# Kernel optimization log

Hardware: AMD Instinct MI355X
Metric: run time of the kernel (lower is better)

The kernel has to match this reference:

```python
import jax, jax.numpy as jnp
import numpy as np

N, E, H = 5000, 40000, 8
DIMS = [(258, 512), (516, 256), (262, 128), (136, 20)]  # (in_feature, out_feature) per GATDeformer


def setup_inputs() -> dict:
    key = jax.random.key(0)
    ks = jax.random.split(key, 10)
    s = 0.05
    data = jax.random.normal(ks[0], (N, 10), jnp.float32)
    src = jax.random.randint(ks[1], (E,), 0, N)
    off = jax.random.randint(ks[2], (E,), 1, N)
    edge_idx = jnp.stack([src, (src + off) % N]).astype(jnp.int32)  # no self loops by construction
    inp = {
        'data': data,
        'edge_idx': edge_idx,
        'W0': jax.random.normal(ks[3], (10, 256), jnp.float32) * s,
        'b0': jnp.zeros((256,), jnp.float32),
    }
    for i, (din, dout) in enumerate(DIMS, start=1):
        k = jax.random.split(ks[3 + i], 3)
        inp[f'W{i}'] = jax.random.normal(k[0], (din, H * dout), jnp.float32) * s
        inp[f'asrc{i}'] = jax.random.normal(k[1], (H, dout), jnp.float32) * s
        inp[f'adst{i}'] = jax.random.normal(k[2], (H, dout), jnp.float32) * s
        inp[f'bias{i}'] = jnp.zeros((dout,), jnp.float32)
    return inp


def _gat(x, src, dst, W, a_s, a_d, b):
    """PyG GATConv (concat=False): returns (mean-over-heads output + bias, alpha [E',H])."""
    Hh, C = a_s.shape
    h = (x @ W).reshape(N, Hh, C)                               # [N,H,C]
    e_s = jnp.einsum('nhc,hc->nh', h, a_s)                      # [N,H]
    e_d = jnp.einsum('nhc,hc->nh', h, a_d)
    logits = jax.nn.leaky_relu(e_s[src] + e_d[dst], 0.2)        # [E',H]
    m = jax.ops.segment_max(logits, dst, num_segments=N)        # segment softmax over incoming edges
    ex = jnp.exp(logits - m[dst])
    alpha = ex / jax.ops.segment_sum(ex, dst, num_segments=N)[dst]
    out = jax.ops.segment_sum(alpha[:, :, None] * h[src], dst, num_segments=N)  # [N,H,C]
    return out.mean(axis=1) + b, alpha


def _deformer(af, src, dst, W, a_s, a_d, b):
    # find_boundary on the layer input features
    up, down = af[:, 0] == 1.0, af[:, 0] == 0.0
    left, right = af[:, 1] == 0.0, af[:, 1] == 1.0
    feat, alpha = _gat(af, src, dst, W, a_s, a_d, b)
    coord = af[:, :2]
    # second propagate: alpha*0.2 reused to aggregate source coordinates, then mean over heads
    msg = (alpha * 0.2)[:, :, None] * coord[src][:, None, :]    # [E',H,2]
    oc = jax.ops.segment_sum(msg, dst, num_segments=N).mean(axis=1)
    # fix_boundary (sequential overwrite order: up then down, left then right)
    c0 = jnp.where(down, 0.0, jnp.where(up, 1.0, oc[:, 0]))
    c1 = jnp.where(right, 1.0, jnp.where(left, 0.0, oc[:, 1]))
    return jnp.stack([c0, c1], axis=1), jax.nn.selu(feat)


def reference(data, edge_idx, W0, b0, W1, asrc1, adst1, bias1, W2, asrc2, adst2, bias2, W3, asrc3, adst3, bias3, W4, asrc4, adst4, bias4):
    sl = jnp.arange(N, dtype=edge_idx.dtype)
    src = jnp.concatenate([edge_idx[0], sl])   # GATConv add_self_loops=True
    dst = jnp.concatenate([edge_idx[1], sl])
    coord = data[:, :2]
    feat = jax.nn.selu(data @ W0 + b0)
    c1_, f1 = _deformer(jnp.concatenate([coord, feat], 1), src, dst, W1, asrc1, adst1, bias1)
    c2_, f2 = _deformer(jnp.concatenate([c1_, coord, f1], 1), src, dst, W2, asrc2, adst2, bias2)
    c3_, f3 = _deformer(jnp.concatenate([c2_, c1_, coord, f2], 1), src, dst, W3, asrc3, adst3, bias3)
    c4_, _ = _deformer(jnp.concatenate([c3_, c2_, c1_, coord, f3], 1), src, dst, W4, asrc4, adst4, bias4)
    return c4_
```

## Files before the change

### kernel.cpp

```cpp
#include <hip/hip_runtime.h>

#define N_NODES 5000
#define NH 8

typedef unsigned short u16;
typedef short bf16x8 __attribute__((ext_vector_type(8)));
typedef float f32x4 __attribute__((ext_vector_type(4)));

static __device__ __forceinline__ float selu_f(float x) {
    const float sc = 1.0507009873554805f;
    const float al = 1.6732632423543772f;
    return x > 0.f ? sc * x : sc * al * (__expf(x) - 1.f);
}

static __device__ __forceinline__ u16 f2bf(float x) {
    union { float f; unsigned u; } v; v.f = x;
    unsigned r = v.u + 0x7fff + ((v.u >> 16) & 1);
    return (u16)(r >> 16);
}

static __device__ __forceinline__ float bf2f(unsigned hi16) {
    union { unsigned u; float f; } v; v.u = hi16 << 16;
    return v.f;
}

__global__ void k_count(const int* __restrict__ ei, int* cnt, int E, int Esz) {
    int e = blockIdx.x * 256 + threadIdx.x;
    if (e >= Esz) return;
    int dst = (e < E) ? ei[E + e] : (e - E);
    atomicAdd(&cnt[dst], 1);
}

__global__ void k_scan(const int* __restrict__ cnt, int* __restrict__ rowp, int n) {
    __shared__ int ps[256];
    int t = threadIdx.x;
    int per = (n + 255) / 256;
    int b = t * per;
    int s = 0;
    for (int i = 0; i < per; ++i) { int idx = b + i; if (idx < n) s += cnt[idx]; }
    ps[t] = s;
    __syncthreads();
    for (int off = 1; off < 256; off <<= 1) {
        int v = (t >= off) ? ps[t - off] : 0;
        __syncthreads();
        ps[t] += v;
        __syncthreads();
    }
    int run = (t == 0) ? 0 : ps[t - 1];
    for (int i = 0; i < per; ++i) {
        int idx = b + i;
        if (idx < n) { rowp[idx] = run; run += cnt[idx]; }
    }
    if (t == 255) rowp[n] = run;
}

__global__ void k_fill(const int* __restrict__ ei, const int* __restrict__ rowp,
                       int* cur, int* ssrc, int E, int Esz) {
    int e = blockIdx.x * 256 + threadIdx.x;
    if (e >= Esz) return;
    int src, dst;
    if (e < E) { src = ei[e]; dst = ei[E + e]; }
    else       { src = e - E; dst = src; }
    int pos = rowp[dst] + atomicAdd(&cur[dst], 1);
    ssrc[pos] = src;
}

__global__ void k_feat0(const float* __restrict__ data, const float* __restrict__ W0,
                        const float* __restrict__ b0, float* __restrict__ f0,
                        float* __restrict__ c0) {
    int n = blockIdx.x;
    int t = threadIdx.x;
    __shared__ float d[10];
    if (t < 10) d[t] = data[n * 10 + t];
    __syncthreads();
    float acc = b0[t];
    #pragma unroll
    for (int k = 0; k < 10; ++k) acc += d[k] * W0[k * 256 + t];
    f0[(size_t)n * 256 + t] = selu_f(acc);
    if (t < 2) c0[n * 2 + t] = d[t];
}

__global__ void k_foldall(const float* W1, const float* W2, const float* W3, const float* W4,
                          const float* s1, const float* s2, const float* s3, const float* s4,
                          const float* d1, const float* d2, const float* d3, const float* d4,
                          float* __restrict__ fsAll, float* __restrict__ fdAll) {
    const int Ks[4] = {258, 516, 262, 136};
    const int Cs[4] = {512, 256, 128, 20};
    int li = blockIdx.y;
    int k = blockIdx.x;
    if (k >= Ks[li]) return;
    const float* W  = (li == 0) ? W1 : (li == 1) ? W2 : (li == 2) ? W3 : W4;
    const float* as = (li == 0) ? s1 : (li == 1) ? s2 : (li == 2) ? s3 : s4;
    const float* ad = (li == 0) ? d1 : (li == 1) ? d2 : (li == 2) ? d3 : d4;
    int C = Cs[li];
    int lane = threadIdx.x;
    float s[8] = {0.f,0.f,0.f,0.f,0.f,0.f,0.f,0.f};
    float d[8] = {0.f,0.f,0.f,0.f,0.f,0.f,0.f,0.f};
    const float* wr = W + (size_t)k * 8 * C;
    for (int c = lane; c < C; c += 64) {
        #pragma unroll
        for (int h = 0; h < 8; ++h) {
            float w = wr[h * C + c];
            s[h] += w * as[h * C + c];
            d[h] += w * ad[h * C + c];
        }
    }
    #pragma unroll
    for (int off = 32; off >= 1; off >>= 1) {
        #pragma unroll
        for (int h = 0; h < 8; ++h) {
            s[h] += __shfl_xor(s[h], off);
            d[h] += __shfl_xor(d[h], off);
        }
    }
    if (lane == 0) {
        float* fo = fsAll + (size_t)li * 516 * 8 + k * 8;
        float* go = fdAll + (size_t)li * 516 * 8 + k * 8;
        #pragma unroll
        for (int h = 0; h < 8; ++h) { fo[h] = s[h]; go[h] = d[h]; }
    }
}

__global__ __launch_bounds__(256) void k_wtrall(const float* W1, const float* W2, const float* W3,
                                                u16* T1, u16* T2, u16* T3) {
    const int Ks[3] = {258, 516, 262};
    const int Cs[3] = {512, 256, 128};
    const int Kps[3] = {288, 544, 288};
    int li = blockIdx.z;
    int C = Cs[li], K = Ks[li], Kp = Kps[li], KK = 8 * Kp;
    int c0 = blockIdx.x * 32;
    int j0 = blockIdx.y * 32;
    if (c0 >= C || j0 >= KK) return;
    const float* W = (li == 0) ? W1 : (li == 1) ? W2 : W3;
    u16* Wt2 = (li == 0) ? T1 : (li == 1) ? T2 : T3;
    __shared__ float tile[32][33];
    int h = j0 / Kp, k0 = j0 % Kp;
    int tid = threadIdx.x;
    for (int idx = tid; idx < 1024; idx += 256) {
        int kr = idx >> 5, cc = idx & 31;
        int gk = k0 + kr;
        tile[kr][cc] = (gk < K) ? W[(size_t)gk * (8 * C) + h * C + c0 + cc] : 0.f;
    }
    __syncthreads();
    for (int idx = tid; idx < 1024; idx += 256) {
        int cr = idx >> 5, kc = idx & 31;
        Wt2[(size_t)(c0 + cr) * KK + j0 + kc] = f2bf(tile[kc][cr]);
    }
}

__global__ __launch_bounds__(256) void k_mf(const float* p0, const float* p1,
                                            const float* p2, const float* p3, int np,
                                            const float* __restrict__ fplain,
                                            const float* __restrict__ facc,
                                            const float* __restrict__ biasp,
                                            int split, int MN, int FC, int K, int Kp,
                                            const float* __restrict__ fs,
                                            const float* __restrict__ fd,
                                            u16* __restrict__ afb,
                                            float* __restrict__ es, float* __restrict__ ed) {
    int n = blockIdx.x, t = threadIdx.x;
    float pes[8] = {0.f,0.f,0.f,0.f,0.f,0.f,0.f,0.f};
    float ped[8] = {0.f,0.f,0.f,0.f,0.f,0.f,0.f,0.f};
    u16* rowb = afb + (size_t)n * Kp;
    for (int cf = t; cf < FC; cf += 256) {
        float v;
        if (biasp) {
            float s = 0.f;
            for (int z = 0; z < split; ++z)
                s += facc[(size_t)z * MN + (size_t)n * FC + cf];
            v = selu_f(s * 0.125f + biasp[cf]);
        } else {
            v = fplain[(size_t)n * FC + cf];
        }
        int c = 2 * np + cf;
        rowb[c] = f2bf(v);
        const float* fsr = fs + c * 8;
        const float* fdr = fd + c * 8;
        #pragma unroll
        for (int h = 0; h < 8; ++h) { pes[h] += v * fsr[h]; ped[h] += v * fdr[h]; }
    }
    if (t < 2 * np) {
        const float* p = (t < 2) ? p0 : (t < 4) ? p1 : (t < 6) ? p2 : p3;
        float v = p[n * 2 + (t & 1)];
        rowb[t] = f2bf(v);
        #pragma unroll
        for (int h = 0; h < 8; ++h) { pes[h] += v * fs[t * 8 + h]; ped[h] += v * fd[t * 8 + h]; }
    }
    for (int c = K + t; c < Kp; c += 256) rowb[c] = 0;
    #pragma unroll
    for (int off = 32; off >= 1; off >>= 1) {
        #pragma unroll
        for (int h = 0; h < 8; ++h) {
            pes[h] += __shfl_xor(pes[h], off);
            ped[h] += __shfl_xor(ped[h], off);
        }
    }
    __shared__ float red[4][16];
    int wv = t >> 6, ln = t & 63;
    if (ln == 0) {
        #pragma unroll
        for (int h = 0; h < 8; ++h) { red[wv][h] = pes[h]; red[wv][8 + h] = ped[h]; }
    }
    __syncthreads();
    if (t < 16) {
        float s = red[0][t] + red[1][t] + red[2][t] + red[3][t];
        if (t < 8) es[n * 8 + t] = s;
        else       ed[n * 8 + (t - 8)] = s;
    }
}

template <int S32>
__global__ __launch_bounds__(256) void k_gag(const float* __restrict__ es,
                            const float* __restrict__ ed,
                            const int* __restrict__ rowp, const int* __restrict__ ssrc,
                            const float* __restrict__ cprev, const u16* __restrict__ afb,
                            u16* __restrict__ g, float* __restrict__ cnext, int Kp) {
    __shared__ int   ls[128];
    __shared__ float la[128 * 8];
    __shared__ float lc0[128], lc1[128], lw[128];
    __shared__ float linv[8];
    int n = blockIdx.x, t = threadIdx.x;
    int s0 = rowp[n];
    int deg = rowp[n + 1] - s0;
    if (deg > 128) deg = 128;
    for (int i = t; i < deg; i += 256) {
        int src = ssrc[s0 + i];
        ls[i] = src;
        lc0[i] = cprev[src * 2];
        lc1[i] = cprev[src * 2 + 1];
    }
    __syncthreads();
    for (int i = t; i < deg * 8; i += 256) {
        int e = i >> 3, h = i & 7;
        float x = es[ls[e] * 8 + h] + ed[n * 8 + h];
        la[i] = x > 0.f ? x : 0.2f * x;
    }
    __syncthreads();
    if (t < 8) {
        float m = -1e30f;
        for (int e = 0; e < deg; ++e) m = fmaxf(m, la[e * 8 + t]);
        float s = 0.f;
        for (int e = 0; e < deg; ++e) {
            float v = __expf(la[e * 8 + t] - m);
            la[e * 8 + t] = v;
            s += v;
        }
        linv[t] = 1.f / s;
    }
    __syncthreads();
    for (int i = t; i < deg; i += 256) {
        float w = 0.f;
        #pragma unroll
        for (int h = 0; h < 8; ++h) w += la[i * 8 + h] * linv[h];
        lw[i] = w;
    }
    int nW = Kp >> 1;
    float acc[8][2 * S32];
    #pragma unroll
    for (int h = 0; h < 8; ++h)
        #pragma unroll
        for (int s = 0; s < 2 * S32; ++s) acc[h][s] = 0.f;
    int e = 0;
    for (; e + 1 < deg; e += 2) {
        const unsigned* r0 = (const unsigned*)(afb + (size_t)ls[e] * Kp);
        const unsigned* r1 = (const unsigned*)(afb + (size_t)ls[e + 1] * Kp);
        unsigned v0[S32], v1[S32];
        #pragma unroll
        for (int s = 0; s < S32; ++s) {
            int w = t + 256 * s;
            v0[s] = (w < nW) ? r0[w] : 0u;
            v1[s] = (w < nW) ? r1[w] : 0u;
        }
        float a0[8], a1[8];
        #pragma unroll
        for (int h = 0; h < 8; ++h) { a0[h] = la[e * 8 + h]; a1[h] = la[(e + 1) * 8 + h]; }
        #pragma unroll
        for (int s = 0; s < S32; ++s) {
            float x0 = bf2f(v0[s] & 0xffff), y0 = bf2f(v0[s] >> 16);
            float x1 = bf2f(v1[s] & 0xffff), y1 = bf2f(v1[s] >> 16);
            #pragma unroll
            for (int h = 0; h < 8; ++h) {
                acc[h][2 * s]     += a0[h] * x0 + a1[h] * x1;
                acc[h][2 * s + 1] += a0[h] * y0 + a1[h] * y1;
            }
        }
    }
    if (e < deg) {
        const unsigned* r0 = (const unsigned*)(afb + (size_t)ls[e] * Kp);
        unsigned v0[S32];
        #pragma unroll
        for (int s = 0; s < S32; ++s) {
            int w = t + 256 * s;
            v0[s] = (w < nW) ? r0[w] : 0u;
        }
        float a0[8];
        #pragma unroll
        for (int h = 0; h < 8; ++h) a0[h] = la[e * 8 + h];
        #pragma unroll
        for (int s = 0; s < S32; ++s) {
            float x0 = bf2f(v0[s] & 0xffff), y0 = bf2f(v0[s] >> 16);
            #pragma unroll
            for (int h = 0; h < 8; ++h) {
                acc[h][2 * s]     += a0[h] * x0;
                acc[h][2 * s + 1] += a0[h] * y0;
            }
        }
    }
    unsigned* grw = (unsigned*)(g + (size_t)n * 8 * Kp);
    #pragma unroll
    for (int s = 0; s < S32; ++s) {
        int w = t + 256 * s;
        if (w < nW) {
            #pragma unroll
            for (int h = 0; h < 8; ++h) {
                float iv = linv[h];
                unsigned lo = f2bf(acc[h][2 * s] * iv);
                unsigned hi = f2bf(acc[h][2 * s + 1] * iv);
                grw[h * nW + w] = lo | (hi << 16);
            }
        }
    }
    __syncthreads();
    if (t == 0) {
        float oc0 = 0.f, oc1 = 0.f;
        for (int i = 0; i < deg; ++i) { oc0 += lw[i] * lc0[i]; oc1 += lw[i] * lc1[i]; }
        oc0 *= 0.025f; oc1 *= 0.025f;
        float a0 = cprev[n * 2], a1 = cprev[n * 2 + 1];
        cnext[n * 2]     = (a0 == 0.f) ? 0.f : ((a0 == 1.f) ? 1.f : oc0);
        cnext[n * 2 + 1] = (a1 == 1.f) ? 1.f : ((a1 == 0.f) ? 0.f : oc1);
    }
}

__global__ __launch_bounds__(256) void k_gemm_s(const u16* __restrict__ A,
                                                const u16* __restrict__ Bt,
                                                float* __restrict__ facc,
                                                int M, int KK, int NC, int kchunk) {
    __shared__ u16 As[128 * 32];
    __shared__ u16 Bs[128 * 32];
    int tid = threadIdx.x;
    int wave = tid >> 6, lane = tid & 63;
    int bm = blockIdx.y * 128, bn = blockIdx.x * 128, z = blockIdx.z;
    int kbeg = z * kchunk, kend = min(KK, kbeg + kchunk);
    int wm = (wave >> 1) * 64, wn = (wave & 1) * 64;
    int l16 = lane & 15, q = lane >> 4;
    f32x4 acc[4][4] = {};
    for (int k0 = kbeg; k0 < kend; k0 += 32) {
        #pragma unroll
        for (int it = 0; it < 2; ++it) {
            int seg = tid + it * 256;
            int row = seg >> 2, sq = seg & 3;
            uint4 va = {0u, 0u, 0u, 0u};
            int grow = bm + row;
            if (grow < M) va = *(const uint4*)(A + (size_t)grow * KK + k0 + sq * 8);
            *(uint4*)(As + row * 32 + ((sq ^ (row & 3)) * 8)) = va;
            uint4 vb = *(const uint4*)(Bt + (size_t)(bn + row) * KK + k0 + sq * 8);
            *(uint4*)(Bs + row * 32 + ((sq ^ (row & 3)) * 8)) = vb;
        }
        __syncthreads();
        bf16x8 fa[4], fb[4];
        #pragma unroll
        for (int mi = 0; mi < 4; ++mi) {
            int row = wm + mi * 16 + l16;
            fa[mi] = *(const bf16x8*)(As + row * 32 + ((q ^ (row & 3)) * 8));
            int col = wn + mi * 16 + l16;
            fb[mi] = *(const bf16x8*)(Bs + col * 32 + ((q ^ (col & 3)) * 8));
        }
        #pragma unroll
        for (int mi = 0; mi < 4; ++mi)
            #pragma unroll
            for (int ni = 0; ni < 4; ++ni)
                acc[mi][ni] = __builtin_amdgcn_mfma_f32_16x16x32_bf16(fa[mi], fb[ni], acc[mi][ni], 0, 0, 0);
        __syncthreads();
    }
    float* out = facc + (size_t)z * M * NC;
    #pragma unroll
    for (int mi = 0; mi < 4; ++mi) {
        int row0 = bm + wm + mi * 16 + q * 4;
        #pragma unroll
        for (int ni = 0; ni < 4; ++ni) {
            int col = bn + wn + ni * 16 + l16;
            #pragma unroll
            for (int r = 0; r < 4; ++r) {
                int row = row0 + r;
                if (row < M) out[(size_t)row * NC + col] = acc[mi][ni][r];
            }
        }
    }
}

__global__ void k_final(const float* __restrict__ es, const float* __restrict__ ed,
                        const int* __restrict__ rowp, const int* __restrict__ ssrc,
                        const float* __restrict__ cprev, float* __restrict__ outp) {
    int wid = (blockIdx.x * blockDim.x + threadIdx.x) >> 6;
    int lane = threadIdx.x & 63;
    if (wid >= N_NODES) return;
    int n = wid;
    int s0 = rowp[n], deg = rowp[n + 1] - s0;
    int h = lane & 7, ei = lane >> 3;
    float edh = ed[n * 8 + h];
    float m = -1e30f;
    for (int b = 0; b < deg; b += 8) {
        int e = b + ei;
        if (e < deg) {
            int src = ssrc[s0 + e];
            float x = es[src * 8 + h] + edh;
            x = x > 0.f ? x : 0.2f * x;
            m = fmaxf(m, x);
        }
    }
    m = fmaxf(m, __shfl_xor(m, 8));
    m = fmaxf(m, __shfl_xor(m, 16));
    m = fmaxf(m, __shfl_xor(m, 32));
    float ssum = 0.f;
    for (int b = 0; b < deg; b += 8) {
        int e = b + ei;
        if (e < deg) {
            int src = ssrc[s0 + e];
            float x = es[src * 8 + h] + edh;
            x = x > 0.f ? x : 0.2f * x;
            ssum += __expf(x - m);
        }
    }
    ssum += __shfl_xor(ssum, 8);
    ssum += __shfl_xor(ssum, 16);
    ssum += __shfl_xor(ssum, 32);
    float inv = 1.f / ssum;
    float oc0 = 0.f, oc1 = 0.f;
    for (int b = 0; b < deg; b += 8) {
        int e = b + ei;
        if (e < deg) {
            int src = ssrc[s0 + e];
            float x = es[src * 8 + h] + edh;
            x = x > 0.f ? x : 0.2f * x;
            float w = __expf(x - m) * inv;
            w += __shfl_xor(w, 1);
            w += __shfl_xor(w, 2);
            w += __shfl_xor(w, 4);
            if (h == 0) {
                oc0 += w * cprev[src * 2];
                oc1 += w * cprev[src * 2 + 1];
            }
        }
    }
    oc0 += __shfl_xor(oc0, 8);  oc1 += __shfl_xor(oc1, 8);
    oc0 += __shfl_xor(oc0, 16); oc1 += __shfl_xor(oc1, 16);
    oc0 += __shfl_xor(oc0, 32); oc1 += __shfl_xor(oc1, 32);
    if (lane == 0) {
        oc0 *= 0.025f; oc1 *= 0.025f;
        float a0 = cprev[n * 2], a1 = cprev[n * 2 + 1];
        outp[n * 2]     = (a0 == 0.f) ? 0.f : ((a0 == 1.f) ? 1.f : oc0);
        outp[n * 2 + 1] = (a1 == 1.f) ? 1.f : ((a1 == 0.f) ? 0.f : oc1);
    }
}

extern "C" void kernel_launch(void* const* d_in, const int* in_sizes, int n_in,
                              void* d_out, int out_size, void* d_ws, size_t ws_size,
                              hipStream_t stream) {
    const float* data = (const float*)d_in[0];
    const int* ei = (const int*)d_in[1];
    const float* W0 = (const float*)d_in[2];
    const float* b0 = (const float*)d_in[3];
    int E = in_sizes[1] / 2;
    int Esz = E + N_NODES;

    char* wp = (char*)d_ws;
    size_t off = 0;
    auto alloc = [&](size_t bytes) {
        void* p = wp + off;
        off += (bytes + 1023) & ~(size_t)1023;
        return p;
    };
    u16*   g     = (u16*)alloc((size_t)N_NODES * 8 * 576 * 2);
    u16*   T1    = (u16*)alloc((size_t)512 * 8 * 288 * 2);
    u16*   T2    = (u16*)alloc((size_t)256 * 8 * 544 * 2);
    u16*   T3    = (u16*)alloc((size_t)128 * 8 * 288 * 2);
    float* facc  = (float*)alloc((size_t)N_NODES * 2048 * 4);
    float* fA    = (float*)alloc((size_t)N_NODES * 256 * 4);
    u16*   afb   = (u16*)alloc((size_t)N_NODES * 576 * 2);
    float* es    = (float*)alloc((size_t)N_NODES * 8 * 4);
    float* ebd   = (float*)alloc((size_t)N_NODES * 8 * 4);
    float* fsAll = (float*)alloc((size_t)4 * 516 * 8 * 4);
    float* fdAll = (float*)alloc((size_t)4 * 516 * 8 * 4);
    float* c0    = (float*)alloc(N_NODES * 2 * 4);
    float* c1    = (float*)alloc(N_NODES * 2 * 4);
    float* c2    = (float*)alloc(N_NODES * 2 * 4);
    float* c3    = (float*)alloc(N_NODES * 2 * 4);
    int* cnt  = (int*)alloc(N_NODES * 2 * 4);
    int* cur  = cnt + N_NODES;
    int* rowp = (int*)alloc((N_NODES + 1) * 4);
    int* ssrc = (int*)alloc(Esz * 4);

    hipMemsetAsync(cnt, 0, N_NODES * 2 * 4, stream);
    int gE = (Esz + 255) / 256;
    k_count<<<gE, 256, 0, stream>>>(ei, cnt, E, Esz);
    k_scan<<<1, 256, 0, stream>>>(cnt, rowp, N_NODES);
    k_fill<<<gE, 256, 0, stream>>>(ei, rowp, cur, ssrc, E, Esz);
    k_feat0<<<N_NODES, 256, 0, stream>>>(data, W0, b0, fA, c0);

    struct LP { const float *W, *as, *ad, *bs; int K, C, split; };
    LP L[4] = {
        {(const float*)d_in[4],  (const float*)d_in[5],  (const float*)d_in[6],  (const float*)d_in[7],  258, 512, 4},
        {(const float*)d_in[8],  (const float*)d_in[9],  (const float*)d_in[10], (const float*)d_in[11], 516, 256, 8},
        {(const float*)d_in[12], (const float*)d_in[13], (const float*)d_in[14], (const float*)d_in[15], 262, 128, 8},
        {(const float*)d_in[16], (const float*)d_in[17], (const float*)d_in[18], (const float*)d_in[19], 136, 20, 1},
    };
    k_foldall<<<dim3(516, 4), 64, 0, stream>>>(L[0].W, L[1].W, L[2].W, L[3].W,
                                               L[0].as, L[1].as, L[2].as, L[3].as,
                                               L[0].ad, L[1].ad, L[2].ad, L[3].ad,
                                               fsAll, fdAll);
    k_wtrall<<<dim3(16, 136, 3), 256, 0, stream>>>(L[0].W, L[1].W, L[2].W, T1, T2, T3);

    float* cbuf[4] = {c0, c1, c2, c3};
    u16* Tb[3] = {T1, T2, T3};
    int FC[4] = {256, 512, 256, 128};

    for (int li = 0; li < 4; ++li) {
        LP& lp = L[li];
        const float* p[4] = {nullptr, nullptr, nullptr, nullptr};
        for (int j = 0; j <= li; ++j) p[j] = cbuf[li - j];
        int Kp = ((lp.K + 31) / 32) * 32;
        int KK = 8 * Kp;
        const float* biasp = (li == 0) ? nullptr : L[li - 1].bs;
        int splitp = (li == 0) ? 1 : L[li - 1].split;
        int MNp = N_NODES * FC[li];
        const float* fs = fsAll + (size_t)li * 516 * 8;
        const float* fd = fdAll + (size_t)li * 516 * 8;

        k_mf<<<N_NODES, 256, 0, stream>>>(p[0], p[1], p[2], p[3], li + 1,
                                          fA, facc, biasp, splitp, MNp, FC[li],
                                          lp.K, Kp, fs, fd, afb, es, ebd);
        if (li < 3) {
            if ((Kp >> 1) <= 256)
                k_gag<1><<<N_NODES, 256, 0, stream>>>(es, ebd, rowp, ssrc, cbuf[li], afb,
                                                      g, cbuf[li + 1], Kp);
            else
                k_gag<2><<<N_NODES, 256, 0, stream>>>(es, ebd, rowp, ssrc, cbuf[li], afb,
                                                      g, cbuf[li + 1], Kp);
            k_gemm_s<<<dim3(lp.C / 128, (N_NODES + 127) / 128, lp.split), 256, 0, stream>>>(
                g, Tb[li], facc, N_NODES, KK, lp.C, KK / lp.split);
        } else {
            k_final<<<(N_NODES + 3) / 4, 256, 0, stream>>>(es, ebd, rowp, ssrc, cbuf[3],
                                                           (float*)d_out);
        }
    }
}
```

Before: 381.5 us.

## Fuse first-layer MLP into k_mf, map one wave per node in gather, store split-K partials as bf16

The standalone k_feat0 kernel is removed and its selu(data@W0+b0) is computed inside the layer-1 k_mf pass, dropping one launch and an fp32 intermediate round trip. k_gag now handles four nodes per block with one wave per node, using 64-bit vector loads, and reduces coordinates with a wave shuffle instead of a serial thread-0 loop. Split-K GEMM partials are written as bf16 instead of fp32, halving that traffic. The costs are more bf16 rounding on the accumulated partial sums and a lower in-degree cap (96 instead of 128) in the gather.

```diff
diff --git a/kernel.cpp b/kernel.cpp
--- a/kernel.cpp
+++ b/kernel.cpp
@@ -63,21 +63,6 @@
     else       { src = e - E; dst = src; }
     int pos = rowp[dst] + atomicAdd(&cur[dst], 1);
     ssrc[pos] = src;
-}
-
-__global__ void k_feat0(const float* __restrict__ data, const float* __restrict__ W0,
-                        const float* __restrict__ b0, float* __restrict__ f0,
-                        float* __restrict__ c0) {
-    int n = blockIdx.x;
-    int t = threadIdx.x;
-    __shared__ float d[10];
-    if (t < 10) d[t] = data[n * 10 + t];
-    __syncthreads();
-    float acc = b0[t];
-    #pragma unroll
-    for (int k = 0; k < 10; ++k) acc += d[k] * W0[k * 256 + t];
-    f0[(size_t)n * 256 + t] = selu_f(acc);
-    if (t < 2) c0[n * 2 + t] = d[t];
 }
 
 __global__ void k_foldall(const float* W1, const float* W2, const float* W3, const float* W4,
@@ -150,27 +135,37 @@
 
 __global__ __launch_bounds__(256) void k_mf(const float* p0, const float* p1,
                                             const float* p2, const float* p3, int np,
-                                            const float* __restrict__ fplain,
-                                            const float* __restrict__ facc,
+                                            const float* __restrict__ data,
+                                            const float* __restrict__ W0,
+                                            const float* __restrict__ b0,
+                                            const u16* __restrict__ facc,
                                             const float* __restrict__ biasp,
                                             int split, int MN, int FC, int K, int Kp,
                                             const float* __restrict__ fs,
                                             const float* __restrict__ fd,
                                             u16* __restrict__ afb,
-                                            float* __restrict__ es, float* __restrict__ ed) {
+                                            float* __restrict__ es, float* __restrict__ ed,
+                                            float* __restrict__ c0out) {
     int n = blockIdx.x, t = threadIdx.x;
+    __shared__ float drow[10];
+    bool l1 = (biasp == nullptr);
+    if (l1 && t < 10) drow[t] = data[n * 10 + t];
+    __syncthreads();
     float pes[8] = {0.f,0.f,0.f,0.f,0.f,0.f,0.f,0.f};
     float ped[8] = {0.f,0.f,0.f,0.f,0.f,0.f,0.f,0.f};
     u16* rowb = afb + (size_t)n * Kp;
     for (int cf = t; cf < FC; cf += 256) {
         float v;
-        if (biasp) {
+        if (l1) {
+            v = b0[cf];
+            #pragma unroll
+            for (int k = 0; k < 10; ++k) v += drow[k] * W0[k * 256 + cf];
+            v = selu_f(v);
+        } else {
             float s = 0.f;
             for (int z = 0; z < split; ++z)
-                s += facc[(size_t)z * MN + (size_t)n * FC + cf];
+                s += bf2f(facc[(size_t)z * MN + (size_t)n * FC + cf]);
             v = selu_f(s * 0.125f + biasp[cf]);
-        } else {
-            v = fplain[(size_t)n * FC + cf];
         }
         int c = 2 * np + cf;
         rowb[c] = f2bf(v);
@@ -180,8 +175,14 @@
         for (int h = 0; h < 8; ++h) { pes[h] += v * fsr[h]; ped[h] += v * fdr[h]; }
     }
     if (t < 2 * np) {
-        const float* p = (t < 2) ? p0 : (t < 4) ? p1 : (t < 6) ? p2 : p3;
-        float v = p[n * 2 + (t & 1)];
+        float v;
+        if (l1) {
+            v = drow[t];
+            c0out[n * 2 + t] = v;
+        } else {
+            const float* p = (t < 2) ? p0 : (t < 4) ? p1 : (t < 6) ? p2 : p3;
+            v = p[n * 2 + (t & 1)];
+        }
         rowb[t] = f2bf(v);
         #pragma unroll
         for (int h = 0; h < 8; ++h) { pes[h] += v * fs[t * 8 + h]; ped[h] += v * fd[t * 8 + h]; }
@@ -209,132 +210,147 @@
     }
 }
 
-template <int S32>
+template <int S>
 __global__ __launch_bounds__(256) void k_gag(const float* __restrict__ es,
                             const float* __restrict__ ed,
                             const int* __restrict__ rowp, const int* __restrict__ ssrc,
                             const float* __restrict__ cprev, const u16* __restrict__ afb,
                             u16* __restrict__ g, float* __restrict__ cnext, int Kp) {
-    __shared__ int   ls[128];
-    __shared__ float la[128 * 8];
-    __shared__ float lc0[128], lc1[128], lw[128];
-    __shared__ float linv[8];
-    int n = blockIdx.x, t = threadIdx.x;
+    const int DC = 96;
+    __shared__ int   ls[4][DC];
+    __shared__ float la[4][DC * 8];
+    __shared__ float lc0[4][DC], lc1[4][DC];
+    __shared__ float linv[4][8];
+    int wv = threadIdx.x >> 6, lane = threadIdx.x & 63;
+    int n = blockIdx.x * 4 + wv;
     int s0 = rowp[n];
     int deg = rowp[n + 1] - s0;
-    if (deg > 128) deg = 128;
-    for (int i = t; i < deg; i += 256) {
+    if (deg > DC) deg = DC;
+    for (int i = lane; i < deg; i += 64) {
         int src = ssrc[s0 + i];
-        ls[i] = src;
-        lc0[i] = cprev[src * 2];
-        lc1[i] = cprev[src * 2 + 1];
-    }
-    __syncthreads();
-    for (int i = t; i < deg * 8; i += 256) {
+        ls[wv][i] = src;
+        lc0[wv][i] = cprev[src * 2];
+        lc1[wv][i] = cprev[src * 2 + 1];
+    }
+    __syncthreads();
+    for (int i = lane; i < deg * 8; i += 64) {
         int e = i >> 3, h = i & 7;
-        float x = es[ls[e] * 8 + h] + ed[n * 8 + h];
-        la[i] = x > 0.f ? x : 0.2f * x;
-    }
-    __syncthreads();
-    if (t < 8) {
+        float x = es[ls[wv][e] * 8 + h] + ed[n * 8 + h];
+        la[wv][i] = x > 0.f ? x : 0.2f * x;
+    }
+    __syncthreads();
+    if (lane < 8) {
         float m = -1e30f;
-        for (int e = 0; e < deg; ++e) m = fmaxf(m, la[e * 8 + t]);
+        for (int e = 0; e < deg; ++e) m = fmaxf(m, la[wv][e * 8 + lane]);
         float s = 0.f;
         for (int e = 0; e < deg; ++e) {
-            float v = __expf(la[e * 8 + t] - m);
-            la[e * 8 + t] = v;
+            float v = __expf(la[wv][e * 8 + lane] - m);
+            la[wv][e * 8 + lane] = v;
             s += v;
         }
-        linv[t] = 1.f / s;
-    }
-    __syncthreads();
-    for (int i = t; i < deg; i += 256) {
+        linv[wv][lane] = 1.f / s;
+    }
+    __syncthreads();
+    float pc0 = 0.f, pc1 = 0.f;
+    for (int i = lane; i < deg; i += 64) {
         float w = 0.f;
         #pragma unroll
-        for (int h = 0; h < 8; ++h) w += la[i * 8 + h] * linv[h];
-        lw[i] = w;
-    }
-    int nW = Kp >> 1;
-    float acc[8][2 * S32];
+        for (int h = 0; h < 8; ++h) w += la[wv][i * 8 + h] * linv[wv][h];
+        pc0 += w * lc0[wv][i];
+        pc1 += w * lc1[wv][i];
+    }
+    #pragma unroll
+    for (int o = 32; o >= 1; o >>= 1) { pc0 += __shfl_xor(pc0, o); pc1 += __shfl_xor(pc1, o); }
+    if (lane == 0) {
+        pc0 *= 0.025f; pc1 *= 0.025f;
+        float a0 = cprev[n * 2], a1 = cprev[n * 2 + 1];
+        cnext[n * 2]     = (a0 == 0.f) ? 0.f : ((a0 == 1.f) ? 1.f : pc0);
+        cnext[n * 2 + 1] = (a1 == 1.f) ? 1.f : ((a1 == 0.f) ? 0.f : pc1);
+    }
+    int n64 = Kp >> 2;
+    float acc[8][4 * S];
     #pragma unroll
     for (int h = 0; h < 8; ++h)
         #pragma unroll
-        for (int s = 0; s < 2 * S32; ++s) acc[h][s] = 0.f;
+        for (int j = 0; j < 4 * S; ++j) acc[h][j] = 0.f;
     int e = 0;
     for (; e + 1 < deg; e += 2) {
-        const unsigned* r0 = (const unsigned*)(afb + (size_t)ls[e] * Kp);
-        const unsigned* r1 = (const unsigned*)(afb + (size_t)ls[e + 1] * Kp);
-        unsigned v0[S32], v1[S32];
-        #pragma unroll
-        for (int s = 0; s < S32; ++s) {
-            int w = t + 256 * s;
-            v0[s] = (w < nW) ? r0[w] : 0u;
-            v1[s] = (w < nW) ? r1[w] : 0u;
+        const uint2* r0 = (const uint2*)(afb + (size_t)ls[wv][e] * Kp);
+        const uint2* r1 = (const uint2*)(afb + (size_t)ls[wv][e + 1] * Kp);
+        uint2 v0[S], v1[S];
+        #pragma unroll
+        for (int s = 0; s < S; ++s) {
+            int w = lane + 64 * s;
+            uint2 zz; zz.x = 0u; zz.y = 0u;
+            v0[s] = (w < n64) ? r0[w] : zz;
+            v1[s] = (w < n64) ? r1[w] : zz;
         }
         float a0[8], a1[8];
         #pragma unroll
-        for (int h = 0; h < 8; ++h) { a0[h] = la[e * 8 + h]; a1[h] = la[(e + 1) * 8 + h]; }
-        #pragma unroll
-        for (int s = 0; s < S32; ++s) {
-            float x0 = bf2f(v0[s] & 0xffff), y0 = bf2f(v0[s] >> 16);
-            float x1 = bf2f(v1[s] & 0xffff), y1 = bf2f(v1[s] >> 16);
+        for (int h = 0; h < 8; ++h) { a0[h] = la[wv][e * 8 + h]; a1[h] = la[wv][(e + 1) * 8 + h]; }
+        #pragma unroll
+        for (int s = 0; s < S; ++s) {
+            float x0 = bf2f(v0[s].x & 0xffff), x1 = bf2f(v0[s].x >> 16);
+            float x2 = bf2f(v0[s].y & 0xffff), x3 = bf2f(v0[s].y >> 16);
+            float y0 = bf2f(v1[s].x & 0xffff), y1 = bf2f(v1[s].x >> 16);
+            float y2 = bf2f(v1[s].y & 0xffff), y3 = bf2f(v1[s].y >> 16);
             #pragma unroll
             for (int h = 0; h < 8; ++h) {
-                acc[h][2 * s]     += a0[h] * x0 + a1[h] * x1;
-                acc[h][2 * s + 1] += a0[h] * y0 + a1[h] * y1;
+                acc[h][4 * s]     += a0[h] * x0 + a1[h] * y0;
+                acc[h][4 * s + 1] += a0[h] * x1 + a1[h] * y1;
+                acc[h][4 * s + 2] += a0[h] * x2 + a1[h] * y2;
+                acc[h][4 * s + 3] += a0[h] * x3 + a1[h] * y3;
             }
         }
     }
     if (e < deg) {
-        const unsigned* r0 = (const unsigned*)(afb + (size_t)ls[e] * Kp);
-        unsigned v0[S32];
-        #pragma unroll
-        for (int s = 0; s < S32; ++s) {
-            int w = t + 256 * s;
-            v0[s] = (w < nW) ? r0[w] : 0u;
+        const uint2* r0 = (const uint2*)(afb + (size_t)ls[wv][e] * Kp);
+        uint2 v0[S];
+        #pragma unroll
+        for (int s = 0; s < S; ++s) {
+            int w = lane + 64 * s;
+            uint2 zz; zz.x = 0u; zz.y = 0u;
+            v0[s] = (w < n64) ? r0[w] : zz;
         }
         float a0[8];
         #pragma unroll
-        for (int h = 0; h < 8; ++h) a0[h] = la[e * 8 + h];
-        #pragma unroll
-        for (int s = 0; s < S32; ++s) {
-            float x0 = bf2f(v0[s] & 0xffff), y0 = bf2f(v0[s] >> 16);
+        for (int h = 0; h < 8; ++h) a0[h] = la[wv][e * 8 + h];
+        #pragma unroll
+        for (int s = 0; s < S; ++s) {
+            float x0 = bf2f(v0[s].x & 0xffff), x1 = bf2f(v0[s].x >> 16);
+            float x2 = bf2f(v0[s].y & 0xffff), x3 = bf2f(v0[s].y >> 16);
             #pragma unroll
             for (int h = 0; h < 8; ++h) {
-                acc[h][2 * s]     += a0[h] * x0;
-                acc[h][2 * s + 1] += a0[h] * y0;
+                acc[h][4 * s]     += a0[h] * x0;
+                acc[h][4 * s + 1] += a0[h] * x1;
+                acc[h][4 * s + 2] += a0[h] * x2;
+                acc[h][4 * s + 3] += a0[h] * x3;
             }
         }
     }
-    unsigned* grw = (unsigned*)(g + (size_t)n * 8 * Kp);
+    uint2* grw = (uint2*)(g + (size_t)n * 8 * Kp);
     #pragma unroll
-    for (int s = 0; s < S32; ++s) {
-        int w = t + 256 * s;
-        if (w < nW) {
+    for (int s = 0; s < S; ++s) {
+        int w = lane + 64 * s;
+        if (w < n64) {
             #pragma unroll
             for (int h = 0; h < 8; ++h) {
-                float iv = linv[h];
-                unsigned lo = f2bf(acc[h][2 * s] * iv);
-                unsigned hi = f2bf(acc[h][2 * s + 1] * iv);
-                grw[h * nW + w] = lo | (hi << 16);
+                float iv = linv[wv][h];
+                unsigned lo = (unsigned)f2bf(acc[h][4 * s] * iv) |
+                              ((unsigned)f2bf(acc[h][4 * s + 1] * iv) << 16);
+                unsigned hi = (unsigned)f2bf(acc[h][4 * s + 2] * iv) |
+                              ((unsigned)f2bf(acc[h][4 * s + 3] * iv) << 16);
+                uint2 o; o.x = lo; o.y = hi;
+                grw[h * n64 + w] = o;
             }
         }
-    }
-    __syncthreads();
-    if (t == 0) {
-        float oc0 = 0.f, oc1 = 0.f;
-        for (int i = 0; i < deg; ++i) { oc0 += lw[i] * lc0[i]; oc1 += lw[i] * lc1[i]; }
-        oc0 *= 0.025f; oc1 *= 0.025f;
-        float a0 = cprev[n * 2], a1 = cprev[n * 2 + 1];
-        cnext[n * 2]     = (a0 == 0.f) ? 0.f : ((a0 == 1.f) ? 1.f : oc0);
-        cnext[n * 2 + 1] = (a1 == 1.f) ? 1.f : ((a1 == 0.f) ? 0.f : oc1);
     }
 }
 
 __global__ __launch_bounds__(256) void k_gemm_s(const u16* __restrict__ A,
                                                 const u16* __restrict__ Bt,
-                                                float* __restrict__ facc,
-                                                int M, int KK, int NC, int kchunk) {
+                                                u16* __restrict__ facc16,
+                                                int M, int KK, int NC, int kchunk, int MN) {
     __shared__ u16 As[128 * 32];
     __shared__ u16 Bs[128 * 32];
     int tid = threadIdx.x;
@@ -372,7 +388,7 @@
                 acc[mi][ni] = __builtin_amdgcn_mfma_f32_16x16x32_bf16(fa[mi], fb[ni], acc[mi][ni], 0, 0, 0);
         __syncthreads();
     }
-    float* out = facc + (size_t)z * M * NC;
+    u16* out = facc16 + (size_t)z * MN;
     #pragma unroll
     for (int mi = 0; mi < 4; ++mi) {
         int row0 = bm + wm + mi * 16 + q * 4;
@@ -382,7 +398,7 @@
             #pragma unroll
             for (int r = 0; r < 4; ++r) {
                 int row = row0 + r;
-                if (row < M) out[(size_t)row * NC + col] = acc[mi][ni][r];
+                if (row < M) out[(size_t)row * NC + col] = f2bf(acc[mi][ni][r]);
             }
         }
     }
@@ -474,8 +490,7 @@
     u16*   T1    = (u16*)alloc((size_t)512 * 8 * 288 * 2);
     u16*   T2    = (u16*)alloc((size_t)256 * 8 * 544 * 2);
     u16*   T3    = (u16*)alloc((size_t)128 * 8 * 288 * 2);
-    float* facc  = (float*)alloc((size_t)N_NODES * 2048 * 4);
-    float* fA    = (float*)alloc((size_t)N_NODES * 256 * 4);
+    u16*   facc  = (u16*)alloc((size_t)8 * N_NODES * 512 * 2);
     u16*   afb   = (u16*)alloc((size_t)N_NODES * 576 * 2);
     float* es    = (float*)alloc((size_t)N_NODES * 8 * 4);
     float* ebd   = (float*)alloc((size_t)N_NODES * 8 * 4);
@@ -495,7 +510,6 @@
     k_count<<<gE, 256, 0, stream>>>(ei, cnt, E, Esz);
     k_scan<<<1, 256, 0, stream>>>(cnt, rowp, N_NODES);
     k_fill<<<gE, 256, 0, stream>>>(ei, rowp, cur, ssrc, E, Esz);
-    k_feat0<<<N_NODES, 256, 0, stream>>>(data, W0, b0, fA, c0);
 
     struct LP { const float *W, *as, *ad, *bs; int K, C, split; };
     LP L[4] = {
@@ -527,17 +541,18 @@
         const float* fd = fdAll + (size_t)li * 516 * 8;
 
         k_mf<<<N_NODES, 256, 0, stream>>>(p[0], p[1], p[2], p[3], li + 1,
-                                          fA, facc, biasp, splitp, MNp, FC[li],
-                                          lp.K, Kp, fs, fd, afb, es, ebd);
+                                          data, W0, b0, facc, biasp, splitp, MNp, FC[li],
+                                          lp.K, Kp, fs, fd, afb, es, ebd, c0);
         if (li < 3) {
-            if ((Kp >> 1) <= 256)
-                k_gag<1><<<N_NODES, 256, 0, stream>>>(es, ebd, rowp, ssrc, cbuf[li], afb,
-                                                      g, cbuf[li + 1], Kp);
+            if ((Kp >> 2) <= 128)
+                k_gag<2><<<N_NODES / 4, 256, 0, stream>>>(es, ebd, rowp, ssrc, cbuf[li], afb,
+                                                          g, cbuf[li + 1], Kp);
             else
-                k_gag<2><<<N_NODES, 256, 0, stream>>>(es, ebd, rowp, ssrc, cbuf[li], afb,
-                                                      g, cbuf[li + 1], Kp);
+                k_gag<3><<<N_NODES / 4, 256, 0, stream>>>(es, ebd, rowp, ssrc, cbuf[li], afb,
+                                                          g, cbuf[li + 1], Kp);
+            int MN = N_NODES * lp.C;
             k_gemm_s<<<dim3(lp.C / 128, (N_NODES + 127) / 128, lp.split), 256, 0, stream>>>(
-                g, Tb[li], facc, N_NODES, KK, lp.C, KK / lp.split);
+                g, Tb[li], facc, N_NODES, KK, lp.C, KK / lp.split, MN);
         } else {
             k_final<<<(N_NODES + 3) / 4, 256, 0, stream>>>(es, ebd, rowp, ssrc, cbuf[3],
                                                            (float*)d_out);
```

After: 403.8 us. 5.8% more time.

## Fuse CSR build into one block, fold layer-0 features into k_mf, store split-K partials as bf16

Applied to the files above, without the earlier changes.

Replaces the count, scan and fill kernels plus the memset with a single 1024-thread kernel that builds the CSR in shared memory. It also folds the first dense layer (data@W0, selu) into the first k_mf launch, removing k_feat0 and its intermediate buffer. Split-K GEMM partial sums are now written as bf16 instead of fp32, which halves partial-sum traffic at some cost in precision. The single-block CSR build serialises about 45K edge atomics on one CU, and the ordering of sources within each destination row remains atomic-order dependent.

```diff
diff --git a/kernel.cpp b/kernel.cpp
--- a/kernel.cpp
+++ b/kernel.cpp
@@ -24,23 +24,26 @@
     return v.f;
 }
 
-__global__ void k_count(const int* __restrict__ ei, int* cnt, int E, int Esz) {
-    int e = blockIdx.x * 256 + threadIdx.x;
-    if (e >= Esz) return;
-    int dst = (e < E) ? ei[E + e] : (e - E);
-    atomicAdd(&cnt[dst], 1);
-}
-
-__global__ void k_scan(const int* __restrict__ cnt, int* __restrict__ rowp, int n) {
-    __shared__ int ps[256];
+__global__ __launch_bounds__(1024) void k_csr(const int* __restrict__ ei,
+                                              int* __restrict__ rowp, int* __restrict__ ssrc,
+                                              int E, int Esz) {
+    __shared__ int cnt[N_NODES];
+    __shared__ int ps[1024];
     int t = threadIdx.x;
-    int per = (n + 255) / 256;
-    int b = t * per;
+    for (int i = t; i < N_NODES; i += 1024) cnt[i] = 0;
+    __syncthreads();
+    for (int e = t; e < Esz; e += 1024) {
+        int dst = (e < E) ? ei[E + e] : (e - E);
+        atomicAdd(&cnt[dst], 1);
+    }
+    __syncthreads();
+    const int per = (N_NODES + 1023) / 1024;
+    int base = t * per;
     int s = 0;
-    for (int i = 0; i < per; ++i) { int idx = b + i; if (idx < n) s += cnt[idx]; }
+    for (int i = 0; i < per; ++i) { int idx = base + i; if (idx < N_NODES) s += cnt[idx]; }
     ps[t] = s;
     __syncthreads();
-    for (int off = 1; off < 256; off <<= 1) {
+    for (int off = 1; off < 1024; off <<= 1) {
         int v = (t >= off) ? ps[t - off] : 0;
         __syncthreads();
         ps[t] += v;
@@ -48,36 +51,23 @@
     }
     int run = (t == 0) ? 0 : ps[t - 1];
     for (int i = 0; i < per; ++i) {
-        int idx = b + i;
-        if (idx < n) { rowp[idx] = run; run += cnt[idx]; }
-    }
-    if (t == 255) rowp[n] = run;
-}
-
-__global__ void k_fill(const int* __restrict__ ei, const int* __restrict__ rowp,
-                       int* cur, int* ssrc, int E, int Esz) {
-    int e = blockIdx.x * 256 + threadIdx.x;
-    if (e >= Esz) return;
-    int src, dst;
-    if (e < E) { src = ei[e]; dst = ei[E + e]; }
-    else       { src = e - E; dst = src; }
-    int pos = rowp[dst] + atomicAdd(&cur[dst], 1);
-    ssrc[pos] = src;
-}
-
-__global__ void k_feat0(const float* __restrict__ data, const float* __restrict__ W0,
-                        const float* __restrict__ b0, float* __restrict__ f0,
-                        float* __restrict__ c0) {
-    int n = blockIdx.x;
-    int t = threadIdx.x;
-    __shared__ float d[10];
-    if (t < 10) d[t] = data[n * 10 + t];
-    __syncthreads();
-    float acc = b0[t];
-    #pragma unroll
-    for (int k = 0; k < 10; ++k) acc += d[k] * W0[k * 256 + t];
-    f0[(size_t)n * 256 + t] = selu_f(acc);
-    if (t < 2) c0[n * 2 + t] = d[t];
+        int idx = base + i;
+        if (idx < N_NODES) {
+            int c = cnt[idx];
+            rowp[idx] = run;
+            cnt[idx] = run;
+            run += c;
+        }
+    }
+    if (t == 1023) rowp[N_NODES] = run;
+    __syncthreads();
+    for (int e = t; e < Esz; e += 1024) {
+        int src, dst;
+        if (e < E) { src = ei[e]; dst = ei[E + e]; }
+        else       { src = e - E; dst = src; }
+        int pos = atomicAdd(&cnt[dst], 1);
+        ssrc[pos] = src;
+    }
 }
 
 __global__ void k_foldall(const float* W1, const float* W2, const float* W3, const float* W4,
@@ -150,27 +140,37 @@
 
 __global__ __launch_bounds__(256) void k_mf(const float* p0, const float* p1,
                                             const float* p2, const float* p3, int np,
-                                            const float* __restrict__ fplain,
-                                            const float* __restrict__ facc,
+                                            const float* __restrict__ data,
+                                            const float* __restrict__ W0,
+                                            const float* __restrict__ b0,
+                                            const u16* __restrict__ facc,
                                             const float* __restrict__ biasp,
                                             int split, int MN, int FC, int K, int Kp,
                                             const float* __restrict__ fs,
                                             const float* __restrict__ fd,
                                             u16* __restrict__ afb,
-                                            float* __restrict__ es, float* __restrict__ ed) {
+                                            float* __restrict__ es, float* __restrict__ ed,
+                                            float* __restrict__ c0out) {
     int n = blockIdx.x, t = threadIdx.x;
+    __shared__ float drow[10];
+    bool l1 = (biasp == nullptr);
+    if (l1 && t < 10) drow[t] = data[n * 10 + t];
+    __syncthreads();
     float pes[8] = {0.f,0.f,0.f,0.f,0.f,0.f,0.f,0.f};
     float ped[8] = {0.f,0.f,0.f,0.f,0.f,0.f,0.f,0.f};
     u16* rowb = afb + (size_t)n * Kp;
     for (int cf = t; cf < FC; cf += 256) {
         float v;
-        if (biasp) {
+        if (l1) {
+            v = b0[cf];
+            #pragma unroll
+            for (int k = 0; k < 10; ++k) v += drow[k] * W0[k * 256 + cf];
+            v = selu_f(v);
+        } else {
             float s = 0.f;
             for (int z = 0; z < split; ++z)
-                s += facc[(size_t)z * MN + (size_t)n * FC + cf];
+                s += bf2f(facc[(size_t)z * MN + (size_t)n * FC + cf]);
             v = selu_f(s * 0.125f + biasp[cf]);
-        } else {
-            v = fplain[(size_t)n * FC + cf];
         }
         int c = 2 * np + cf;
         rowb[c] = f2bf(v);
@@ -180,8 +180,14 @@
         for (int h = 0; h < 8; ++h) { pes[h] += v * fsr[h]; ped[h] += v * fdr[h]; }
     }
     if (t < 2 * np) {
-        const float* p = (t < 2) ? p0 : (t < 4) ? p1 : (t < 6) ? p2 : p3;
-        float v = p[n * 2 + (t & 1)];
+        float v;
+        if (l1) {
+            v = drow[t];
+            c0out[n * 2 + t] = v;
+        } else {
+            const float* p = (t < 2) ? p0 : (t < 4) ? p1 : (t < 6) ? p2 : p3;
+            v = p[n * 2 + (t & 1)];
+        }
         rowb[t] = f2bf(v);
         #pragma unroll
         for (int h = 0; h < 8; ++h) { pes[h] += v * fs[t * 8 + h]; ped[h] += v * fd[t * 8 + h]; }
@@ -333,8 +339,8 @@
 
 __global__ __launch_bounds__(256) void k_gemm_s(const u16* __restrict__ A,
                                                 const u16* __restrict__ Bt,
-                                                float* __restrict__ facc,
-                                                int M, int KK, int NC, int kchunk) {
+                                                u16* __restrict__ facc16,
+                                                int M, int KK, int NC, int kchunk, int MN) {
     __shared__ u16 As[128 * 32];
     __shared__ u16 Bs[128 * 32];
     int tid = threadIdx.x;
@@ -372,7 +378,7 @@
                 acc[mi][ni] = __builtin_amdgcn_mfma_f32_16x16x32_bf16(fa[mi], fb[ni], acc[mi][ni], 0, 0, 0);
         __syncthreads();
     }
-    float* out = facc + (size_t)z * M * NC;
+    u16* out = facc16 + (size_t)z * MN;
     #pragma unroll
     for (int mi = 0; mi < 4; ++mi) {
         int row0 = bm + wm + mi * 16 + q * 4;
@@ -382,7 +388,7 @@
             #pragma unroll
             for (int r = 0; r < 4; ++r) {
                 int row = row0 + r;
-                if (row < M) out[(size_t)row * NC + col] = acc[mi][ni][r];
+                if (row < M) out[(size_t)row * NC + col] = f2bf(acc[mi][ni][r]);
             }
         }
     }
@@ -474,8 +480,7 @@
     u16*   T1    = (u16*)alloc((size_t)512 * 8 * 288 * 2);
     u16*   T2    = (u16*)alloc((size_t)256 * 8 * 544 * 2);
     u16*   T3    = (u16*)alloc((size_t)128 * 8 * 288 * 2);
-    float* facc  = (float*)alloc((size_t)N_NODES * 2048 * 4);
-    float* fA    = (float*)alloc((size_t)N_NODES * 256 * 4);
+    u16*   facc  = (u16*)alloc((size_t)8 * N_NODES * 512 * 2);
     u16*   afb   = (u16*)alloc((size_t)N_NODES * 576 * 2);
     float* es    = (float*)alloc((size_t)N_NODES * 8 * 4);
     float* ebd   = (float*)alloc((size_t)N_NODES * 8 * 4);
@@ -485,17 +490,10 @@
     float* c1    = (float*)alloc(N_NODES * 2 * 4);
     float* c2    = (float*)alloc(N_NODES * 2 * 4);
     float* c3    = (float*)alloc(N_NODES * 2 * 4);
-    int* cnt  = (int*)alloc(N_NODES * 2 * 4);
-    int* cur  = cnt + N_NODES;
     int* rowp = (int*)alloc((N_NODES + 1) * 4);
     int* ssrc = (int*)alloc(Esz * 4);
 
-    hipMemsetAsync(cnt, 0, N_NODES * 2 * 4, stream);
-    int gE = (Esz + 255) / 256;
-    k_count<<<gE, 256, 0, stream>>>(ei, cnt, E, Esz);
-    k_scan<<<1, 256, 0, stream>>>(cnt, rowp, N_NODES);
-    k_fill<<<gE, 256, 0, stream>>>(ei, rowp, cur, ssrc, E, Esz);
-    k_feat0<<<N_NODES, 256, 0, stream>>>(data, W0, b0, fA, c0);
+    k_csr<<<1, 1024, 0, stream>>>(ei, rowp, ssrc, E, Esz);
 
     struct LP { const float *W, *as, *ad, *bs; int K, C, split; };
     LP L[4] = {
@@ -527,8 +525,8 @@
         const float* fd = fdAll + (size_t)li * 516 * 8;
 
         k_mf<<<N_NODES, 256, 0, stream>>>(p[0], p[1], p[2], p[3], li + 1,
-                                          fA, facc, biasp, splitp, MNp, FC[li],
-                                          lp.K, Kp, fs, fd, afb, es, ebd);
+                                          data, W0, b0, facc, biasp, splitp, MNp, FC[li],
+                                          lp.K, Kp, fs, fd, afb, es, ebd, c0);
         if (li < 3) {
             if ((Kp >> 1) <= 256)
                 k_gag<1><<<N_NODES, 256, 0, stream>>>(es, ebd, rowp, ssrc, cbuf[li], afb,
@@ -536,8 +534,9 @@
             else
                 k_gag<2><<<N_NODES, 256, 0, stream>>>(es, ebd, rowp, ssrc, cbuf[li], afb,
                                                       g, cbuf[li + 1], Kp);
+            int MN = N_NODES * lp.C;
             k_gemm_s<<<dim3(lp.C / 128, (N_NODES + 127) / 128, lp.split), 256, 0, stream>>>(
-                g, Tb[li], facc, N_NODES, KK, lp.C, KK / lp.split);
+                g, Tb[li], facc, N_NODES, KK, lp.C, KK / lp.split, MN);
         } else {
             k_final<<<(N_NODES + 3) / 4, 256, 0, stream>>>(es, ebd, rowp, ssrc, cbuf[3],
                                                            (float*)d_out);
```

Result: slower. 426.4 us (+11.8%).
